# Kernel tuning notes

Measured on AMD Instinct MI355X. Metric: run time of the kernel, lower is better.

Reference implementation:

```python
import jax, jax.numpy as jnp
import numpy as np

DIM = 192
WIN = 8
HEADS = 6
HEAD_DIM = DIM // HEADS
SCALE = HEAD_DIM ** -0.5
N = WIN * WIN


def _relative_position_index():
    coords = np.stack(np.meshgrid(np.arange(WIN), np.arange(WIN), indexing='ij'))  # [2,W,W]
    flat = coords.reshape(2, -1)  # [2,N]
    rel = flat[:, :, None] - flat[:, None, :]  # [2,N,N]
    rel = rel.transpose(1, 2, 0)
    rel[:, :, 0] += WIN - 1
    rel[:, :, 1] += WIN - 1
    rel[:, :, 0] *= 2 * WIN - 1
    return rel.sum(-1).astype(np.int32)  # [N,N]


def setup_inputs() -> dict:
    key = jax.random.key(0)
    ks = jax.random.split(key, 6)
    B = 4096
    x = jax.random.normal(ks[0], (B, N, DIM), dtype=jnp.float32)
    qkv_w = jax.random.normal(ks[1], (3 * DIM, DIM), dtype=jnp.float32) * (DIM ** -0.5)
    qkv_b = jnp.zeros((3 * DIM,), dtype=jnp.float32)
    proj_w = jax.random.normal(ks[2], (DIM, DIM), dtype=jnp.float32) * (DIM ** -0.5)
    proj_b = jnp.zeros((DIM,), dtype=jnp.float32)
    num_rel = (2 * WIN - 1) * (2 * WIN - 1)
    bias_table = jax.random.normal(ks[3], (num_rel, HEADS), dtype=jnp.float32) * 0.02
    rel_idx = jnp.asarray(_relative_position_index())
    return {"x": x, "qkv_w": qkv_w, "qkv_b": qkv_b, "proj_w": proj_w,
            "proj_b": proj_b, "bias_table": bias_table, "rel_idx": rel_idx}


def reference(x, qkv_w, qkv_b, proj_w, proj_b, bias_table, rel_idx):
    B, n, C = x.shape
    qkv = x @ qkv_w.T + qkv_b  # [B,N,3C]
    qkv = qkv.reshape(B, n, 3, HEADS, HEAD_DIM).transpose(2, 0, 3, 1, 4)  # [3,B,H,N,hd]
    q, k, v = qkv[0], qkv[1], qkv[2]
    attn = jnp.einsum('bhnd,bhmd->bhnm', q * SCALE, k)  # [B,H,N,N]
    bias = bias_table[rel_idx]  # [N,N,H]
    attn = attn + bias.transpose(2, 0, 1)[None]  # add [1,H,N,N]
    attn = jax.nn.softmax(attn, axis=-1)
    out = jnp.einsum('bhnm,bhmd->bhnd', attn, v)
    out = out.transpose(0, 2, 1, 3).reshape(B, n, C)
    return out @ proj_w.T + proj_b
```

## Files before the change

### kernel.cpp

```cpp
#include <hip/hip_runtime.h>

#define NTOK 64
#define DIM 192
#define HEADS 6
#define HD 32
#define SCALE 0.17677669529663687f
#define XSS 200

typedef __bf16 bf16x8 __attribute__((ext_vector_type(8)));
typedef float f32x4 __attribute__((ext_vector_type(4)));

union U8 { bf16x8 v; unsigned short s[8]; };
union F4 { float4 v; float f[4]; };

__device__ __forceinline__ unsigned short f2bf(float f) {
  union { float f; unsigned u; } v; v.f = f;
  unsigned u = v.u;
  return (unsigned short)((u + 0x7FFFu + ((u >> 16) & 1u)) >> 16);
}

__global__ void prep_kernel(const float* __restrict__ qkv_w,
                            const float* __restrict__ proj_w,
                            const float* __restrict__ bias_table,
                            const int* __restrict__ rel_idx,
                            unsigned short* __restrict__ wq,
                            unsigned short* __restrict__ wp,
                            float* __restrict__ biasf) {
  int i = blockIdx.x * 256 + threadIdx.x;
  if (i < 3 * DIM * DIM) wq[i] = f2bf(qkv_w[i]);
  if (i < DIM * DIM) wp[i] = f2bf(proj_w[i]);
  if (i < HEADS * NTOK * NTOK) {
    int h = i >> 12;
    int nm = i & 4095;
    biasf[i] = bias_table[rel_idx[nm] * HEADS + h];
  }
}

__global__ __launch_bounds__(384) void attn_kernel(
    const float* __restrict__ x,
    const float* __restrict__ qkv_b,
    const float* __restrict__ proj_b,
    const unsigned short* __restrict__ wq,
    const unsigned short* __restrict__ wp,
    const float* __restrict__ biasf,
    float* __restrict__ out) {
  __shared__ unsigned short xs[NTOK * XSS];

  const int tid = threadIdx.x;
  const int w = tid >> 6;
  const int lane = tid & 63;
  const int l15 = lane & 15;
  const int quad = lane >> 4;
  const long b = blockIdx.x;
  const int h = w;

  {
    const float4* xg = (const float4*)(x + b * (NTOK * DIM));
    #pragma unroll
    for (int it = 0; it < 8; ++it) {
      int idx = tid + it * 384;
      float4 v = xg[idx];
      int row = idx / 48;
      int col = (idx % 48) * 4;
      ushort4 o;
      o.x = f2bf(v.x); o.y = f2bf(v.y); o.z = f2bf(v.z); o.w = f2bf(v.w);
      *(ushort4*)&xs[row * XSS + col] = o;
    }
  }
  __syncthreads();

  const int prm = ((l15 >> 2) << 3) | (l15 & 3);
  const f32x4 zero = {0.f, 0.f, 0.f, 0.f};

  bf16x8 qfrag[4];
  {
    const unsigned short* wqh = wq + ((size_t)h * 32) * DIM;
    F4 qb0, qb1;
    qb0.v = *(const float4*)(qkv_b + h * 32 + quad * 8);
    qb1.v = *(const float4*)(qkv_b + h * 32 + quad * 8 + 4);
    #pragma unroll
    for (int nt = 0; nt < 4; ++nt) {
      bf16x8 xn[6];
      #pragma unroll
      for (int ks = 0; ks < 6; ++ks)
        xn[ks] = *(const bf16x8*)&xs[(nt * 16 + l15) * XSS + ks * 32 + quad * 8];
      f32x4 a0 = zero, a1 = zero;
      #pragma unroll
      for (int ks = 0; ks < 6; ++ks) {
        bf16x8 w0 = *(const bf16x8*)(wqh + (size_t)(prm + 0) * DIM + ks * 32 + quad * 8);
        bf16x8 w1 = *(const bf16x8*)(wqh + (size_t)(prm + 4) * DIM + ks * 32 + quad * 8);
        a0 = __builtin_amdgcn_mfma_f32_16x16x32_bf16(w0, xn[ks], a0, 0, 0, 0);
        a1 = __builtin_amdgcn_mfma_f32_16x16x32_bf16(w1, xn[ks], a1, 0, 0, 0);
      }
      U8 t;
      #pragma unroll
      for (int g = 0; g < 4; ++g) {
        t.s[g]     = f2bf((a0[g] + qb0.f[g]) * SCALE);
        t.s[4 + g] = f2bf((a1[g] + qb1.f[g]) * SCALE);
      }
      qfrag[nt] = t.v;
    }
  }

  bf16x8 kfrag[4];
  U8 vbu[2][2];
  {
    const unsigned short* wkh = wq + ((size_t)(192 + h * 32)) * DIM;
    const unsigned short* wvh = wq + ((size_t)(384 + h * 32)) * DIM;
    F4 kb0, kb1;
    kb0.v = *(const float4*)(qkv_b + 192 + h * 32 + quad * 8);
    kb1.v = *(const float4*)(qkv_b + 192 + h * 32 + quad * 8 + 4);
    const float vbias0 = qkv_b[384 + h * 32 + l15];
    const float vbias1 = qkv_b[384 + h * 32 + 16 + l15];
    #pragma unroll
    for (int mt = 0; mt < 4; ++mt) {
      const int kv = mt >> 1, half = mt & 1;
      const int xrow = kv * 32 + half * 4 + prm;
      bf16x8 xp[6];
      #pragma unroll
      for (int ks = 0; ks < 6; ++ks)
        xp[ks] = *(const bf16x8*)&xs[xrow * XSS + ks * 32 + quad * 8];
      f32x4 ka0 = zero, ka1 = zero, va0 = zero, va1 = zero;
      #pragma unroll
      for (int ks = 0; ks < 6; ++ks) {
        bf16x8 wk0 = *(const bf16x8*)(wkh + (size_t)(prm + 0) * DIM + ks * 32 + quad * 8);
        bf16x8 wk1 = *(const bf16x8*)(wkh + (size_t)(prm + 4) * DIM + ks * 32 + quad * 8);
        bf16x8 wv0 = *(const bf16x8*)(wvh + (size_t)(l15 + 0) * DIM + ks * 32 + quad * 8);
        bf16x8 wv1 = *(const bf16x8*)(wvh + (size_t)(l15 + 16) * DIM + ks * 32 + quad * 8);
        ka0 = __builtin_amdgcn_mfma_f32_16x16x32_bf16(wk0, xp[ks], ka0, 0, 0, 0);
        ka1 = __builtin_amdgcn_mfma_f32_16x16x32_bf16(wk1, xp[ks], ka1, 0, 0, 0);
        va0 = __builtin_amdgcn_mfma_f32_16x16x32_bf16(xp[ks], wv0, va0, 0, 0, 0);
        va1 = __builtin_amdgcn_mfma_f32_16x16x32_bf16(xp[ks], wv1, va1, 0, 0, 0);
      }
      U8 t;
      #pragma unroll
      for (int g = 0; g < 4; ++g) {
        t.s[g]     = f2bf(ka0[g] + kb0.f[g]);
        t.s[4 + g] = f2bf(ka1[g] + kb1.f[g]);
        vbu[0][kv].s[half * 4 + g] = f2bf(va0[g] + vbias0);
        vbu[1][kv].s[half * 4 + g] = f2bf(va1[g] + vbias1);
      }
      kfrag[mt] = t.v;
    }
  }

  f32x4 s[4][4];
  #pragma unroll
  for (int mt = 0; mt < 4; ++mt)
    #pragma unroll
    for (int nt = 0; nt < 4; ++nt)
      s[mt][nt] = __builtin_amdgcn_mfma_f32_16x16x32_bf16(kfrag[mt], qfrag[nt], zero, 0, 0, 0);

  bf16x8 pa[4][2];
  {
    const float* bh = biasf + h * 4096;
    #pragma unroll
    for (int nt = 0; nt < 4; ++nt) {
      float ve[16];
      #pragma unroll
      for (int mt = 0; mt < 4; ++mt) {
        F4 bb;
        bb.v = *(const float4*)(bh + (nt * 16 + l15) * 64 + (mt >> 1) * 32 + quad * 8 + (mt & 1) * 4);
        #pragma unroll
        for (int g = 0; g < 4; ++g) ve[mt * 4 + g] = s[mt][nt][g] + bb.f[g];
      }
      float mx = ve[0];
      #pragma unroll
      for (int t = 1; t < 16; ++t) mx = fmaxf(mx, ve[t]);
      mx = fmaxf(mx, __shfl_xor(mx, 16));
      mx = fmaxf(mx, __shfl_xor(mx, 32));
      float sm = 0.f;
      #pragma unroll
      for (int t = 0; t < 16; ++t) { ve[t] = __expf(ve[t] - mx); sm += ve[t]; }
      sm += __shfl_xor(sm, 16);
      sm += __shfl_xor(sm, 32);
      float r = __builtin_amdgcn_rcpf(sm);
      U8 t0, t1;
      #pragma unroll
      for (int j = 0; j < 8; ++j) {
        t0.s[j] = f2bf(ve[j] * r);
        t1.s[j] = f2bf(ve[8 + j] * r);
      }
      pa[nt][0] = t0.v;
      pa[nt][1] = t1.v;
    }
  }

  f32x4 o[4][2];
  #pragma unroll
  for (int nt = 0; nt < 4; ++nt)
    #pragma unroll
    for (int c2 = 0; c2 < 2; ++c2) {
      f32x4 acc = __builtin_amdgcn_mfma_f32_16x16x32_bf16(pa[nt][0], vbu[c2][0].v, zero, 0, 0, 0);
      o[nt][c2] = __builtin_amdgcn_mfma_f32_16x16x32_bf16(pa[nt][1], vbu[c2][1].v, acc, 0, 0, 0);
    }

  __syncthreads();
  #pragma unroll
  for (int nt = 0; nt < 4; ++nt)
    #pragma unroll
    for (int c2 = 0; c2 < 2; ++c2)
      #pragma unroll
      for (int g = 0; g < 4; ++g)
        xs[(nt * 16 + quad * 4 + g) * XSS + h * 32 + c2 * 16 + l15] = f2bf(o[nt][c2][g]);
  __syncthreads();

  {
    bf16x8 af[4][6];
    #pragma unroll
    for (int nt = 0; nt < 4; ++nt)
      #pragma unroll
      for (int ks = 0; ks < 6; ++ks)
        af[nt][ks] = *(const bf16x8*)&xs[(nt * 16 + l15) * XSS + ks * 32 + quad * 8];
    float* og = out + b * (NTOK * DIM);
    #pragma unroll
    for (int i = 0; i < 2; ++i) {
      const int e = w * 32 + i * 16 + l15;
      f32x4 acc[4] = {zero, zero, zero, zero};
      #pragma unroll
      for (int ks = 0; ks < 6; ++ks) {
        bf16x8 bw = *(const bf16x8*)(wp + (size_t)e * DIM + ks * 32 + quad * 8);
        #pragma unroll
        for (int nt = 0; nt < 4; ++nt)
          acc[nt] = __builtin_amdgcn_mfma_f32_16x16x32_bf16(af[nt][ks], bw, acc[nt], 0, 0, 0);
      }
      const float pb = proj_b[e];
      #pragma unroll
      for (int nt = 0; nt < 4; ++nt)
        #pragma unroll
        for (int g = 0; g < 4; ++g)
          og[(nt * 16 + quad * 4 + g) * DIM + e] = acc[nt][g] + pb;
    }
  }
}

extern "C" void kernel_launch(void* const* d_in, const int* in_sizes, int n_in,
                              void* d_out, int out_size, void* d_ws, size_t ws_size,
                              hipStream_t stream) {
  const float* x          = (const float*)d_in[0];
  const float* qkv_w      = (const float*)d_in[1];
  const float* qkv_b      = (const float*)d_in[2];
  const float* proj_w     = (const float*)d_in[3];
  const float* proj_b     = (const float*)d_in[4];
  const float* bias_table = (const float*)d_in[5];
  const int*   rel_idx    = (const int*)d_in[6];

  unsigned short* wq = (unsigned short*)d_ws;
  unsigned short* wp = wq + 3 * DIM * DIM;
  float* biasf = (float*)(wp + DIM * DIM);

  prep_kernel<<<432, 256, 0, stream>>>(qkv_w, proj_w, bias_table, rel_idx, wq, wp, biasf);
  attn_kernel<<<4096, 384, 0, stream>>>(x, qkv_b, proj_b, wq, wp, biasf, (float*)d_out);
}
```

Before: 523.0 us.

## Use native bf16 converts, fold log2e, seed MFMA with bias, drop softmax max

Replaces the manual round-to-nearest bf16 bit conversion with native __bf16 casts, which the compiler can lower to hardware convert instructions. It folds log2(e) into the Q scale and the relative-position bias so the softmax can use exp2 directly. It loads the bias as the MFMA accumulator's initial value, removing a separate add pass. It also drops the row-max subtraction and its cross-lane shuffles, cutting VALU and shuffle work in the softmax at the cost of overflow safety if the logits get large.

```diff
diff --git a/kernel.cpp b/kernel.cpp
--- a/kernel.cpp
+++ b/kernel.cpp
@@ -5,19 +5,14 @@
 #define HEADS 6
 #define HD 32
 #define SCALE 0.17677669529663687f
+#define LOG2E 1.4426950408889634f
 #define XSS 200
 
 typedef __bf16 bf16x8 __attribute__((ext_vector_type(8)));
+typedef __bf16 bf16x4 __attribute__((ext_vector_type(4)));
 typedef float f32x4 __attribute__((ext_vector_type(4)));
 
-union U8 { bf16x8 v; unsigned short s[8]; };
 union F4 { float4 v; float f[4]; };
-
-__device__ __forceinline__ unsigned short f2bf(float f) {
-  union { float f; unsigned u; } v; v.f = f;
-  unsigned u = v.u;
-  return (unsigned short)((u + 0x7FFFu + ((u >> 16) & 1u)) >> 16);
-}
 
 __global__ void prep_kernel(const float* __restrict__ qkv_w,
                             const float* __restrict__ proj_w,
@@ -27,12 +22,12 @@
                             unsigned short* __restrict__ wp,
                             float* __restrict__ biasf) {
   int i = blockIdx.x * 256 + threadIdx.x;
-  if (i < 3 * DIM * DIM) wq[i] = f2bf(qkv_w[i]);
-  if (i < DIM * DIM) wp[i] = f2bf(proj_w[i]);
+  if (i < 3 * DIM * DIM) ((__bf16*)wq)[i] = (__bf16)qkv_w[i];
+  if (i < DIM * DIM) ((__bf16*)wp)[i] = (__bf16)proj_w[i];
   if (i < HEADS * NTOK * NTOK) {
     int h = i >> 12;
     int nm = i & 4095;
-    biasf[i] = bias_table[rel_idx[nm] * HEADS + h];
+    biasf[i] = bias_table[rel_idx[nm] * HEADS + h] * LOG2E;
   }
 }
 
@@ -62,15 +57,17 @@
       float4 v = xg[idx];
       int row = idx / 48;
       int col = (idx % 48) * 4;
-      ushort4 o;
-      o.x = f2bf(v.x); o.y = f2bf(v.y); o.z = f2bf(v.z); o.w = f2bf(v.w);
-      *(ushort4*)&xs[row * XSS + col] = o;
+      bf16x4 o;
+      o[0] = (__bf16)v.x; o[1] = (__bf16)v.y;
+      o[2] = (__bf16)v.z; o[3] = (__bf16)v.w;
+      *(bf16x4*)&xs[row * XSS + col] = o;
     }
   }
   __syncthreads();
 
   const int prm = ((l15 >> 2) << 3) | (l15 & 3);
   const f32x4 zero = {0.f, 0.f, 0.f, 0.f};
+  const float qsc = SCALE * LOG2E;
 
   bf16x8 qfrag[4];
   {
@@ -78,6 +75,9 @@
     F4 qb0, qb1;
     qb0.v = *(const float4*)(qkv_b + h * 32 + quad * 8);
     qb1.v = *(const float4*)(qkv_b + h * 32 + quad * 8 + 4);
+    float qb0s[4], qb1s[4];
+    #pragma unroll
+    for (int g = 0; g < 4; ++g) { qb0s[g] = qb0.f[g] * qsc; qb1s[g] = qb1.f[g] * qsc; }
     #pragma unroll
     for (int nt = 0; nt < 4; ++nt) {
       bf16x8 xn[6];
@@ -92,18 +92,18 @@
         a0 = __builtin_amdgcn_mfma_f32_16x16x32_bf16(w0, xn[ks], a0, 0, 0, 0);
         a1 = __builtin_amdgcn_mfma_f32_16x16x32_bf16(w1, xn[ks], a1, 0, 0, 0);
       }
-      U8 t;
+      bf16x8 t;
       #pragma unroll
       for (int g = 0; g < 4; ++g) {
-        t.s[g]     = f2bf((a0[g] + qb0.f[g]) * SCALE);
-        t.s[4 + g] = f2bf((a1[g] + qb1.f[g]) * SCALE);
-      }
-      qfrag[nt] = t.v;
+        t[g]     = (__bf16)fmaf(a0[g], qsc, qb0s[g]);
+        t[4 + g] = (__bf16)fmaf(a1[g], qsc, qb1s[g]);
+      }
+      qfrag[nt] = t;
     }
   }
 
   bf16x8 kfrag[4];
-  U8 vbu[2][2];
+  bf16x8 vbu[2][2];
   {
     const unsigned short* wkh = wq + ((size_t)(192 + h * 32)) * DIM;
     const unsigned short* wvh = wq + ((size_t)(384 + h * 32)) * DIM;
@@ -132,58 +132,52 @@
         va0 = __builtin_amdgcn_mfma_f32_16x16x32_bf16(xp[ks], wv0, va0, 0, 0, 0);
         va1 = __builtin_amdgcn_mfma_f32_16x16x32_bf16(xp[ks], wv1, va1, 0, 0, 0);
       }
-      U8 t;
+      bf16x8 t;
       #pragma unroll
       for (int g = 0; g < 4; ++g) {
-        t.s[g]     = f2bf(ka0[g] + kb0.f[g]);
-        t.s[4 + g] = f2bf(ka1[g] + kb1.f[g]);
-        vbu[0][kv].s[half * 4 + g] = f2bf(va0[g] + vbias0);
-        vbu[1][kv].s[half * 4 + g] = f2bf(va1[g] + vbias1);
-      }
-      kfrag[mt] = t.v;
-    }
-  }
-
+        t[g]     = (__bf16)(ka0[g] + kb0.f[g]);
+        t[4 + g] = (__bf16)(ka1[g] + kb1.f[g]);
+        vbu[0][kv][half * 4 + g] = (__bf16)(va0[g] + vbias0);
+        vbu[1][kv][half * 4 + g] = (__bf16)(va1[g] + vbias1);
+      }
+      kfrag[mt] = t;
+    }
+  }
+
+  const float* bh = biasf + h * 4096;
   f32x4 s[4][4];
   #pragma unroll
   for (int mt = 0; mt < 4; ++mt)
     #pragma unroll
-    for (int nt = 0; nt < 4; ++nt)
-      s[mt][nt] = __builtin_amdgcn_mfma_f32_16x16x32_bf16(kfrag[mt], qfrag[nt], zero, 0, 0, 0);
+    for (int nt = 0; nt < 4; ++nt) {
+      f32x4 binit = *(const f32x4*)(bh + (nt * 16 + l15) * 64 +
+                                    (mt >> 1) * 32 + quad * 8 + (mt & 1) * 4);
+      s[mt][nt] = __builtin_amdgcn_mfma_f32_16x16x32_bf16(kfrag[mt], qfrag[nt], binit, 0, 0, 0);
+    }
 
   bf16x8 pa[4][2];
-  {
-    const float* bh = biasf + h * 4096;
-    #pragma unroll
-    for (int nt = 0; nt < 4; ++nt) {
-      float ve[16];
-      #pragma unroll
-      for (int mt = 0; mt < 4; ++mt) {
-        F4 bb;
-        bb.v = *(const float4*)(bh + (nt * 16 + l15) * 64 + (mt >> 1) * 32 + quad * 8 + (mt & 1) * 4);
-        #pragma unroll
-        for (int g = 0; g < 4; ++g) ve[mt * 4 + g] = s[mt][nt][g] + bb.f[g];
-      }
-      float mx = ve[0];
-      #pragma unroll
-      for (int t = 1; t < 16; ++t) mx = fmaxf(mx, ve[t]);
-      mx = fmaxf(mx, __shfl_xor(mx, 16));
-      mx = fmaxf(mx, __shfl_xor(mx, 32));
-      float sm = 0.f;
-      #pragma unroll
-      for (int t = 0; t < 16; ++t) { ve[t] = __expf(ve[t] - mx); sm += ve[t]; }
-      sm += __shfl_xor(sm, 16);
-      sm += __shfl_xor(sm, 32);
-      float r = __builtin_amdgcn_rcpf(sm);
-      U8 t0, t1;
-      #pragma unroll
-      for (int j = 0; j < 8; ++j) {
-        t0.s[j] = f2bf(ve[j] * r);
-        t1.s[j] = f2bf(ve[8 + j] * r);
-      }
-      pa[nt][0] = t0.v;
-      pa[nt][1] = t1.v;
-    }
+  #pragma unroll
+  for (int nt = 0; nt < 4; ++nt) {
+    float p[16];
+    #pragma unroll
+    for (int t = 0; t < 16; ++t)
+      p[t] = __builtin_amdgcn_exp2f(s[t >> 2][nt][t & 3]);
+    float s0 = (p[0] + p[1]) + (p[2] + p[3]);
+    float s1 = (p[4] + p[5]) + (p[6] + p[7]);
+    float s2 = (p[8] + p[9]) + (p[10] + p[11]);
+    float s3 = (p[12] + p[13]) + (p[14] + p[15]);
+    float sm = (s0 + s1) + (s2 + s3);
+    sm += __shfl_xor(sm, 16);
+    sm += __shfl_xor(sm, 32);
+    float r = __builtin_amdgcn_rcpf(sm);
+    bf16x8 t0, t1;
+    #pragma unroll
+    for (int j = 0; j < 8; ++j) {
+      t0[j] = (__bf16)(p[j] * r);
+      t1[j] = (__bf16)(p[8 + j] * r);
+    }
+    pa[nt][0] = t0;
+    pa[nt][1] = t1;
   }
 
   f32x4 o[4][2];
@@ -191,8 +185,8 @@
   for (int nt = 0; nt < 4; ++nt)
     #pragma unroll
     for (int c2 = 0; c2 < 2; ++c2) {
-      f32x4 acc = __builtin_amdgcn_mfma_f32_16x16x32_bf16(pa[nt][0], vbu[c2][0].v, zero, 0, 0, 0);
-      o[nt][c2] = __builtin_amdgcn_mfma_f32_16x16x32_bf16(pa[nt][1], vbu[c2][1].v, acc, 0, 0, 0);
+      f32x4 acc = __builtin_amdgcn_mfma_f32_16x16x32_bf16(pa[nt][0], vbu[c2][0], zero, 0, 0, 0);
+      o[nt][c2] = __builtin_amdgcn_mfma_f32_16x16x32_bf16(pa[nt][1], vbu[c2][1], acc, 0, 0, 0);
     }
 
   __syncthreads();
@@ -202,7 +196,8 @@
     for (int c2 = 0; c2 < 2; ++c2)
       #pragma unroll
       for (int g = 0; g < 4; ++g)
-        xs[(nt * 16 + quad * 4 + g) * XSS + h * 32 + c2 * 16 + l15] = f2bf(o[nt][c2][g]);
+        *(__bf16*)&xs[(nt * 16 + quad * 4 + g) * XSS + h * 32 + c2 * 16 + l15] =
+            (__bf16)o[nt][c2][g];
   __syncthreads();
 
   {
```

Result: no change. 526.6 us (+0.7%).
